# Optimization experiments

Hardware: AMD Instinct MI355X
Metric: run time of the kernel (lower is better)

Reference implementation:

```python
import jax, jax.numpy as jnp
import numpy as np

# ---- module config (init_kwargs) ----
B, CIN, H, W_ = 2, 64, 56, 56
COUT, KH, KW = 128, 3, 3
K = CIN * KH * KW               # 576, reduction dim
ARRAY_ROWS = 128
IN_SLICES = (2, 2, 2, 2)        # 8-bit inputs, 2-bit slices
W_SLICES = (2, 2, 2, 2)         # 8-bit weights, 2-bit slices
N_STEPS_IN = 2 ** sum(IN_SLICES)    # 256, unsigned quantizer
N_STEPS_W = 2 ** sum(W_SLICES)      # 256
ADC_BINS = 256
ADC_STEP = 4.0

def _shifts_masks(slices):
    masks, shifts = [], [0]
    for s in slices[::-1]:
        masks.append((1 << s) - 1)
        shifts.append(s + shifts[-1])
    return np.array(shifts[-2::-1], np.int32), np.array(masks[::-1], np.int32)

_ish, _im = _shifts_masks(IN_SLICES)
_wsh, _wm = _shifts_masks(W_SLICES)
ISH, IM = jnp.asarray(_ish), jnp.asarray(_im)
WSH, WM = jnp.asarray(_wsh), jnp.asarray(_wm)
ISF = jnp.asarray((1 << _ish).astype(np.float32))  # slice recombine weights 2^shift
WSF = jnp.asarray((1 << _wsh).astype(np.float32))


def setup_inputs() -> dict:
    key = jax.random.key(0)
    k1, k2 = jax.random.split(key)
    return {
        "x": jax.random.normal(k1, (B, CIN, H, W_), jnp.float32),
        "w": jax.random.normal(k2, (COUT, CIN, KH, KW), jnp.float32),
    }


def _im2col(x):
    # 3x3 SAME conv patches, ordering [Cin, kh, kw] to match w.reshape(COUT, K)
    xp = jnp.pad(x, ((0, 0), (0, 0), (1, 1), (1, 1)))
    cols = jnp.stack([xp[:, :, i:i + H, j:j + W_]
                      for i in range(KH) for j in range(KW)], axis=2)  # [B,Cin,9,H,W]
    return cols.transpose(0, 3, 4, 1, 2).reshape(B * H * W_, K)  # [Nx, K]


def _quant_unsigned(v, n_steps):
    # Quantizer.offset + Quantizer.forward (unsigned, per-row over dim=-1)
    offs = v.min(axis=-1, keepdims=True)
    vr = v - offs
    step = vr.max(axis=-1, keepdims=True) / (n_steps - 1)
    q = jnp.round(jnp.clip(vr, 0.0, step * n_steps) / step).astype(jnp.int32)
    return q, step[..., 0], offs[..., 0]


def _slice_bits(q, shifts, masks):
    # Slicer.forward: stack (q >> shift) & mask along new leading slice dim
    s = shifts.reshape((-1,) + (1,) * q.ndim)
    m = masks.reshape((-1,) + (1,) * q.ndim)
    return (q[None] >> s) & m


def _chunk(t):
    # Chunker.forward over last dim K
    nb = -(-K // ARRAY_ROWS)
    npb = -(-K // nb)
    pad = nb * npb - K
    t = jnp.pad(t, [(0, 0)] * (t.ndim - 1) + [(0, pad)])
    t = t.reshape(t.shape[:-1] + (nb, npb))
    return jnp.moveaxis(t, -2, 0)  # [nb, ..., npb]


def reference(x, w):
    xf = _im2col(x)                    # [Nx, K]
    wf = w.reshape(COUT, K)            # [Ny, K]
    x_sum = xf.sum(axis=-1)            # [Nx]
    w_sum = wf.sum(axis=-1)            # [Ny]

    xq, x_scale, x_offs = _quant_unsigned(xf, N_STEPS_IN)
    wq, w_scale, w_offs = _quant_unsigned(wf, N_STEPS_W)

    xc = _chunk(_slice_bits(xq, ISH, IM))  # [nb, nis, Nx, npb] int32
    wc = _chunk(_slice_bits(wq, WSH, WM))  # [nb, nws, Ny, npb] int32

    # bit-serial crossbar MACs per (chunk, weight-slice, input-slice)
    z = jnp.einsum('bixk,bwyk->bwixy',
                   xc.astype(jnp.float32), wc.astype(jnp.float32))  # [nb,nws,nis,Nx,Ny]

    # ADC digitization (unsigned, fixed step): quantize then dequantize
    z = jnp.round(jnp.clip(z, 0.0, ADC_STEP * ADC_BINS) / ADC_STEP) * ADC_STEP

    # Chunker.reverse: sum crossbar blocks; Slicer.reverse: shift-weighted sums
    z = z.sum(axis=0)                               # [nws,nis,Nx,Ny]
    z = jnp.einsum('wixy,w,i->xy', z, WSF, ISF)     # [Nx,Ny]

    # dequantize scales and unsigned-offset correction:
    # x.y = sx*sy*(xq.yq) + x_offs*sum(y) + y_offs*sum(x) - x_offs*y_offs*K
    z = z * x_scale[:, None] * w_scale[None, :]
    z = (z + x_offs[:, None] * w_sum[None, :]
           + w_offs[None, :] * x_sum[:, None]
           - x_offs[:, None] * w_offs[None, :] * K)

    return z.reshape(B, H, W_, COUT).transpose(0, 3, 1, 2)  # [B,Cout,H,W]
```

## Files before the change

### kernel.cpp

```cpp
#include <hip/hip_runtime.h>


#define NXROW 6272
#define KDIM  576
#define NPB   116
#define SSTR  656

typedef int i32x4 __attribute__((ext_vector_type(4)));
typedef float f32x4 __attribute__((ext_vector_type(4)));

__device__ __forceinline__ i32x4 slice2b(i32x4 v, int sh) {
    i32x4 r;
    r[0] = (int)(((unsigned)v[0] >> sh) & 0x03030303u);
    r[1] = (int)(((unsigned)v[1] >> sh) & 0x03030303u);
    r[2] = (int)(((unsigned)v[2] >> sh) & 0x03030303u);
    r[3] = (int)(((unsigned)v[3] >> sh) & 0x03030303u);
    return r;
}

__global__ __launch_bounds__(256) void k_q(
    const float* __restrict__ x, const float* __restrict__ w,
    unsigned char* __restrict__ Xq, unsigned char* __restrict__ Wq,
    float* __restrict__ xsc, float* __restrict__ xof, float* __restrict__ xsm,
    float* __restrict__ wsc, float* __restrict__ wof, float* __restrict__ wsm)
{
    __shared__ __align__(16) unsigned char scr[4][SSTR];

    int tid = threadIdx.x, wv = tid >> 6, lane = tid & 63;
    int W = blockIdx.x * 4 + wv;
    unsigned char* myrow = scr[wv];

    if (lane < 16) {
        int col = lane < 12 ? (lane / 3) * 128 + 116 + (lane % 3) * 4
                            : 624 + (lane - 12) * 4;
        *(unsigned int*)(myrow + col) = 0u;
    }

    float v[9];
    unsigned char* dstbase;
    int rl;
    float *sc, *of, *sm;
    int sidx;

    if (W < NXROW) {
        int b = W >= 3136 ? 1 : 0;
        int pos = W - b * 3136;
        int hg = pos / 56, wg = pos - hg * 56;
        const float* xb = x + (size_t)(b * 64) * 3136;
#pragma unroll
        for (int r = 0; r < 9; r++) {
            int k = r * 64 + lane;
            int cin = k / 9;
            int off = k - cin * 9;
            int kh = off / 3;
            int kw = off - kh * 3;
            int hr = hg - 1 + kh, wc = wg - 1 + kw;
            bool ok = ((unsigned)hr < 56u) && ((unsigned)wc < 56u);
            v[r] = ok ? xb[cin * 3136 + hr * 56 + wc] : 0.f;
        }
        dstbase = Xq + (size_t)(W >> 4) * 10240;  rl = W & 15;
        sc = xsc; of = xof; sm = xsm; sidx = W;
    } else {
        int row = W - NXROW;
        const float* wr = w + (size_t)row * KDIM;
#pragma unroll
        for (int r = 0; r < 9; r++) v[r] = wr[r * 64 + lane];
        dstbase = Wq + (size_t)(row >> 4) * 10240;  rl = row & 15;
        sc = wsc; of = wof; sm = wsm; sidx = row;
    }

    float mn = v[0], mx = v[0], s = 0.f;
#pragma unroll
    for (int r = 0; r < 9; r++) { mn = fminf(mn, v[r]); mx = fmaxf(mx, v[r]); s += v[r]; }
#pragma unroll
    for (int off2 = 1; off2 < 64; off2 <<= 1) {
        mn = fminf(mn, __shfl_xor(mn, off2));
        mx = fmaxf(mx, __shfl_xor(mx, off2));
        s += __shfl_xor(s, off2);
    }
    float step = (mx - mn) / 255.0f;
    if (lane == 0) { sc[sidx] = step; of[sidx] = mn; sm[sidx] = s; }

#pragma unroll
    for (int r = 0; r < 9; r++) {
        int q = (int)rintf((v[r] - mn) / step);
        q = q < 0 ? 0 : (q > 255 ? 255 : q);
        int k = r * 64 + lane;
        int ch = k / NPB;
        myrow[k + 12 * ch] = (unsigned char)q;
    }
    __syncthreads();

    if (lane < 40) {
        int u = lane;
        i32x4 seg = *(const i32x4*)(myrow + u * 16);
        int dst16 = (u >> 3) * 128 + ((u >> 2) & 1) * 64 + (u & 3) * 16 + rl;
        *(i32x4*)(dstbase + (size_t)dst16 * 16) = seg;
    }
}

__device__ __forceinline__ void chunk_ws(const unsigned char* xt, const unsigned char* wt,
                                         int ch, int lane, i32x4 (&acc4)[4])
{
    const i32x4 zero = {0, 0, 0, 0};
    i32x4 x0 = *(const i32x4*)(xt + ch * 2048 + lane * 16);
    i32x4 x1 = *(const i32x4*)(xt + ch * 2048 + 1024 + lane * 16);
    i32x4 w0 = *(const i32x4*)(wt + ch * 2048 + lane * 16);
    i32x4 w1 = *(const i32x4*)(wt + ch * 2048 + 1024 + lane * 16);
    i32x4 ws0[4], ws1[4];
#pragma unroll
    for (int ws = 0; ws < 4; ws++) {
        ws0[ws] = slice2b(w0, 6 - 2 * ws);
        ws1[ws] = slice2b(w1, 6 - 2 * ws);
    }
#pragma unroll
    for (int is = 0; is < 4; is++) {
        int ish = 6 - 2 * is;
        i32x4 a0 = slice2b(x0, ish), a1 = slice2b(x1, ish);
#pragma unroll
        for (int ws = 0; ws < 4; ws++) {
            i32x4 d = __builtin_amdgcn_mfma_i32_16x16x64_i8(ws0[ws], a0, zero, 0, 0, 0);
            d = __builtin_amdgcn_mfma_i32_16x16x64_i8(ws1[ws], a1, d, 0, 0, 0);
            int sh = ish + 6 - 2 * ws;
#pragma unroll
            for (int r = 0; r < 4; r++) {
                int z = d[r];
                z = z > 1024 ? 1024 : z;
                int t = (z >> 2) & 1;
                int r4 = (z + 1 + t) & ~3;
                acc4[ws][r] += r4 << sh;
            }
        }
    }
}

__global__ __launch_bounds__(256) void k_d(
    const unsigned char* __restrict__ Xq, const unsigned char* __restrict__ Wq,
    const float* __restrict__ xscg, const float* __restrict__ xofg,
    const float* __restrict__ xsmg,
    const float* __restrict__ wscg, const float* __restrict__ wofg,
    const float* __restrict__ wsmg, float* __restrict__ out)
{
    __shared__ __align__(16) int pacc[2][64][4];

    int tid = threadIdx.x, wv = tid >> 6, lane = tid & 63;
    int g = lane >> 4, i16 = lane & 15;
    int blk = blockIdx.x;
    int ct = blk & 7, rp = blk >> 3;
    int tl = wv & 1, khalf = wv >> 1;
    int rtile = rp * 2 + tl;
    const unsigned char* xt = Xq + (size_t)rtile * 10240;
    const unsigned char* wt = Wq + (size_t)ct * 10240;

    i32x4 acc4[4] = {{0,0,0,0},{0,0,0,0},{0,0,0,0},{0,0,0,0}};
    if (khalf == 0) {
        chunk_ws(xt, wt, 0, lane, acc4);
        chunk_ws(xt, wt, 1, lane, acc4);
        chunk_ws(xt, wt, 2, lane, acc4);
    } else {
        chunk_ws(xt, wt, 3, lane, acc4);
        chunk_ws(xt, wt, 4, lane, acc4);
    }
    i32x4 acc;
#pragma unroll
    for (int r = 0; r < 4; r++)
        acc[r] = (acc4[0][r] + acc4[1][r]) + (acc4[2][r] + acc4[3][r]);

    if (khalf == 0) *(i32x4*)&pacc[tl][lane][0] = acc;
    __syncthreads();

    if (khalf == 1) {
        i32x4 p = *(const i32x4*)&pacc[tl][lane][0];
#pragma unroll
        for (int r = 0; r < 4; r++) acc[r] += p[r];

        int b = rtile >= 196 ? 1 : 0;
        int xrow = rtile * 16 + i16;
        float xs_ = xscg[xrow], xo = xofg[xrow], xsv = xsmg[xrow];
        int hw = (rtile - 196 * b) * 16 + i16;
#pragma unroll
        for (int r = 0; r < 4; r++) {
            int wrow = ct * 16 + g * 4 + r;
            float tt = ((float)acc[r] * xs_) * wscg[wrow];
            float res = ((tt + xo * wsmg[wrow]) + wofg[wrow] * xsv)
                      - (xo * wofg[wrow]) * 576.0f;
            out[(size_t)(b * 128 + wrow) * 3136 + hw] = res;
        }
    }
}

extern "C" void kernel_launch(void* const* d_in, const int* in_sizes, int n_in,
                              void* d_out, int out_size, void* d_ws, size_t ws_size,
                              hipStream_t stream) {
    const float* x = (const float*)d_in[0];
    const float* w = (const float*)d_in[1];
    float* out = (float*)d_out;

    unsigned char* Xq = (unsigned char*)d_ws;
    unsigned char* Wq = Xq + (size_t)392 * 10240;
    float* xsc = (float*)(Wq + 8 * 10240);
    float* xof = xsc + NXROW;
    float* xsm = xof + NXROW;
    float* wsc = xsm + NXROW;
    float* wof = wsc + 128;
    float* wsm = wof + 128;

    hipLaunchKernelGGL(k_q, dim3(1600), dim3(256), 0, stream,
                       x, w, Xq, Wq, xsc, xof, xsm, wsc, wof, wsm);
    hipLaunchKernelGGL(k_d, dim3(1568), dim3(256), 0, stream,
                       Xq, Wq, xsc, xof, xsm, wsc, wof, wsm, out);
}
```

Measured before the change: 33.90 us.

## Stage 16 im2col rows per block in LDS for coalesced quantization

The quantize kernel now handles 16 activation rows per block instead of one row per wavefront. Threads are mapped so that the 16 consecutive spatial positions are adjacent lanes, which makes the global reads of x coalesced. The raw values are transposed through padded LDS, and each row is then quantized by 16 lanes that pack bytes into dword stores. The output tile is written as contiguous 16-byte stores. This adds LDS usage (about 49KB per block) and two barriers, and cuts the grid from 1600 to 424 blocks, which may reduce occupancy.

```diff
diff --git a/kernel.cpp b/kernel.cpp
--- a/kernel.cpp
+++ b/kernel.cpp
@@ -7,7 +7,6 @@
 #define SSTR  656
 
 typedef int i32x4 __attribute__((ext_vector_type(4)));
-typedef float f32x4 __attribute__((ext_vector_type(4)));
 
 __device__ __forceinline__ i32x4 slice2b(i32x4 v, int sh) {
     i32x4 r;
@@ -18,84 +17,127 @@
     return r;
 }
 
+__device__ __forceinline__ void quant36(const float (&v)[36], unsigned char* rowp,
+                                        int i16, float* scp, float* ofp, float* smp)
+{
+    {
+        int col = i16 < 12 ? (i16 / 3) * 128 + 116 + (i16 % 3) * 4
+                           : 624 + (i16 - 12) * 4;
+        *(unsigned int*)(rowp + col) = 0u;
+    }
+    float mn = v[0], mx = v[0], sm = 0.f;
+#pragma unroll
+    for (int m = 0; m < 36; m++) { mn = fminf(mn, v[m]); mx = fmaxf(mx, v[m]); sm += v[m]; }
+#pragma unroll
+    for (int off = 1; off < 16; off <<= 1) {
+        mn = fminf(mn, __shfl_xor(mn, off));
+        mx = fmaxf(mx, __shfl_xor(mx, off));
+        sm += __shfl_xor(sm, off);
+    }
+    float step = (mx - mn) / 255.0f;
+    if (i16 == 0) { *scp = step; *ofp = mn; *smp = sm; }
+    int k0 = i16 * 36;
+#pragma unroll
+    for (int d = 0; d < 9; d++) {
+        unsigned int dw = 0;
+#pragma unroll
+        for (int mb = 0; mb < 4; mb++) {
+            int q = (int)rintf((v[d * 4 + mb] - mn) / step);
+            q = q < 0 ? 0 : (q > 255 ? 255 : q);
+            dw |= (unsigned)q << (8 * mb);
+        }
+        int kd = k0 + d * 4;
+        int ch = kd / NPB;
+        *(unsigned int*)(rowp + kd + 12 * ch) = dw;
+    }
+}
+
 __global__ __launch_bounds__(256) void k_q(
     const float* __restrict__ x, const float* __restrict__ w,
     unsigned char* __restrict__ Xq, unsigned char* __restrict__ Wq,
     float* __restrict__ xsc, float* __restrict__ xof, float* __restrict__ xsm,
     float* __restrict__ wsc, float* __restrict__ wof, float* __restrict__ wsm)
 {
-    __shared__ __align__(16) unsigned char scr[4][SSTR];
+    __shared__ float rawf[576 * 17];
+    __shared__ __align__(16) unsigned char qrow[16 * SSTR];
 
     int tid = threadIdx.x, wv = tid >> 6, lane = tid & 63;
-    int W = blockIdx.x * 4 + wv;
-    unsigned char* myrow = scr[wv];
-
-    if (lane < 16) {
-        int col = lane < 12 ? (lane / 3) * 128 + 116 + (lane % 3) * 4
-                            : 624 + (lane - 12) * 4;
-        *(unsigned int*)(myrow + col) = 0u;
-    }
-
-    float v[9];
-    unsigned char* dstbase;
-    int rl;
-    float *sc, *of, *sm;
-    int sidx;
-
-    if (W < NXROW) {
-        int b = W >= 3136 ? 1 : 0;
-        int pos = W - b * 3136;
+    int blk = blockIdx.x;
+
+    if (blk < 392) {
+        int row = tid & 15;
+        int R = blk * 16 + row;
+        int b = R >= 3136 ? 1 : 0;
+        int pos = R - b * 3136;
         int hg = pos / 56, wg = pos - hg * 56;
         const float* xb = x + (size_t)(b * 64) * 3136;
-#pragma unroll
-        for (int r = 0; r < 9; r++) {
-            int k = r * 64 + lane;
+        int kbase = tid >> 4;
+#pragma unroll
+        for (int it = 0; it < 36; it++) {
+            int k = kbase + it * 16;
             int cin = k / 9;
             int off = k - cin * 9;
-            int kh = off / 3;
-            int kw = off - kh * 3;
+            int kh = off / 3, kw = off - kh * 3;
             int hr = hg - 1 + kh, wc = wg - 1 + kw;
             bool ok = ((unsigned)hr < 56u) && ((unsigned)wc < 56u);
-            v[r] = ok ? xb[cin * 3136 + hr * 56 + wc] : 0.f;
-        }
-        dstbase = Xq + (size_t)(W >> 4) * 10240;  rl = W & 15;
-        sc = xsc; of = xof; sm = xsm; sidx = W;
+            rawf[k * 17 + row] = ok ? xb[cin * 3136 + hr * 56 + wc] : 0.f;
+        }
+        __syncthreads();
+
+        int i16 = lane & 15;
+        int r = wv * 4 + (lane >> 4);
+        float v[36];
+#pragma unroll
+        for (int j = 0; j < 36; j++)
+            v[j] = rawf[(i16 * 36 + j) * 17 + r];
+        quant36(v, qrow + r * SSTR, i16,
+                xsc + blk * 16 + r, xof + blk * 16 + r, xsm + blk * 16 + r);
+        __syncthreads();
+
+        unsigned char* dst = Xq + (size_t)blk * 10240;
+        for (int s = tid; s < 640; s += 256) {
+            int rl = s & 15;
+            int u = (s >> 7) * 8 + ((s >> 6) & 1) * 4 + ((s >> 4) & 3);
+            *(i32x4*)(dst + (size_t)s * 16) = *(const i32x4*)(&qrow[rl * SSTR + u * 16]);
+        }
     } else {
-        int row = W - NXROW;
+        int row = (blk - 392) * 4 + wv;
+        unsigned char* myrow = qrow + wv * SSTR;
+        if (lane < 16) {
+            int col = lane < 12 ? (lane / 3) * 128 + 116 + (lane % 3) * 4
+                                : 624 + (lane - 12) * 4;
+            *(unsigned int*)(myrow + col) = 0u;
+        }
         const float* wr = w + (size_t)row * KDIM;
+        float v[9];
 #pragma unroll
         for (int r = 0; r < 9; r++) v[r] = wr[r * 64 + lane];
-        dstbase = Wq + (size_t)(row >> 4) * 10240;  rl = row & 15;
-        sc = wsc; of = wof; sm = wsm; sidx = row;
-    }
-
-    float mn = v[0], mx = v[0], s = 0.f;
-#pragma unroll
-    for (int r = 0; r < 9; r++) { mn = fminf(mn, v[r]); mx = fmaxf(mx, v[r]); s += v[r]; }
-#pragma unroll
-    for (int off2 = 1; off2 < 64; off2 <<= 1) {
-        mn = fminf(mn, __shfl_xor(mn, off2));
-        mx = fmaxf(mx, __shfl_xor(mx, off2));
-        s += __shfl_xor(s, off2);
-    }
-    float step = (mx - mn) / 255.0f;
-    if (lane == 0) { sc[sidx] = step; of[sidx] = mn; sm[sidx] = s; }
-
-#pragma unroll
-    for (int r = 0; r < 9; r++) {
-        int q = (int)rintf((v[r] - mn) / step);
-        q = q < 0 ? 0 : (q > 255 ? 255 : q);
-        int k = r * 64 + lane;
-        int ch = k / NPB;
-        myrow[k + 12 * ch] = (unsigned char)q;
-    }
-    __syncthreads();
-
-    if (lane < 40) {
-        int u = lane;
-        i32x4 seg = *(const i32x4*)(myrow + u * 16);
-        int dst16 = (u >> 3) * 128 + ((u >> 2) & 1) * 64 + (u & 3) * 16 + rl;
-        *(i32x4*)(dstbase + (size_t)dst16 * 16) = seg;
+        float mn = v[0], mx = v[0], s = 0.f;
+#pragma unroll
+        for (int r = 0; r < 9; r++) { mn = fminf(mn, v[r]); mx = fmaxf(mx, v[r]); s += v[r]; }
+#pragma unroll
+        for (int off2 = 1; off2 < 64; off2 <<= 1) {
+            mn = fminf(mn, __shfl_xor(mn, off2));
+            mx = fmaxf(mx, __shfl_xor(mx, off2));
+            s += __shfl_xor(s, off2);
+        }
+        float step = (mx - mn) / 255.0f;
+        if (lane == 0) { wsc[row] = step; wof[row] = mn; wsm[row] = s; }
+#pragma unroll
+        for (int r = 0; r < 9; r++) {
+            int q = (int)rintf((v[r] - mn) / step);
+            q = q < 0 ? 0 : (q > 255 ? 255 : q);
+            int k = r * 64 + lane;
+            int ch = k / NPB;
+            myrow[k + 12 * ch] = (unsigned char)q;
+        }
+        __syncthreads();
+        if (lane < 40) {
+            int u = lane;
+            i32x4 seg = *(const i32x4*)(myrow + u * 16);
+            int dst16 = (u >> 3) * 128 + ((u >> 2) & 1) * 64 + (u & 3) * 16 + (row & 15);
+            *(i32x4*)(Wq + (size_t)(row >> 4) * 10240 + (size_t)dst16 * 16) = seg;
+        }
     }
 }
 
@@ -205,7 +247,7 @@
     float* wof = wsc + 128;
     float* wsm = wof + 128;
 
-    hipLaunchKernelGGL(k_q, dim3(1600), dim3(256), 0, stream,
+    hipLaunchKernelGGL(k_q, dim3(424), dim3(256), 0, stream,
                        x, w, Xq, Wq, xsc, xof, xsm, wsc, wof, wsm);
     hipLaunchKernelGGL(k_d, dim3(1568), dim3(256), 0, stream,
                        Xq, Wq, xsc, xof, xsm, wsc, wof, wsm, out);
```

Measured after the change: 41.84 us. +23.4%, slower.
